# Kernel optimization log

Measured on AMD Instinct MI355X. Metric: run time of the kernel, lower is better.

Reference implementation:

```python
import jax, jax.numpy as jnp
import numpy as np

LN_EPS = 1e-5

def layer_norm(x, gamma, beta):
    mu = jnp.mean(x, axis=-1, keepdims=True)
    var = jnp.mean(jnp.square(x - mu), axis=-1, keepdims=True)
    return (x - mu) * jax.lax.rsqrt(var + LN_EPS) * gamma + beta

def setup_inputs() -> dict:
    key = jax.random.key(0)
    ks = jax.random.split(key, 10)
    B, C, N = 8, 256, 4096
    s = 1.0 / np.sqrt(C)
    inp = {
        "x": jax.random.normal(ks[0], (B, C, N), dtype=jnp.float32),
        "W_qkv": jax.random.uniform(ks[1], (C, C), jnp.float32, -s, s),            # Linear(dim, dim, bias=False)
        "W_mlp": jax.random.uniform(ks[2], (2 * C, 2 * C), jnp.float32, -0.5 * s, 0.5 * s),
        "b_mlp": jax.random.uniform(ks[3], (2 * C,), jnp.float32, -0.5 * s, 0.5 * s),
        "g1": jnp.ones((4 * C,), jnp.float32),
        "beta1": jnp.zeros((4 * C,), jnp.float32),
        "W_res": jax.random.uniform(ks[4], (C, 4 * C), jnp.float32, -0.25 * s, 0.25 * s),  # Linear(4*dim, dim, bias=False)
        "g2": jnp.ones((C,), jnp.float32),
        "beta2": jnp.zeros((C,), jnp.float32),
    }
    return inp

def reference(x, W_qkv, W_mlp, b_mlp, g1, beta1, W_res, g2, beta2):
    # x: (B, C, N) channels-first -> (B, N, C)
    NITER = 2  # niter_heads
    x = jnp.swapaxes(x, 1, 2)
    x = x @ W_qkv.T                                   # shared_qkv, (B, N, C)
    v = jax.lax.stop_gradient(x)                      # x.clone().detach()
    for _ in range(NITER):
        # first_context = x^T @ v : (B, C, C)
        ctx = jnp.einsum('bnc,bnd->bcd', x, v)
        out = jax.nn.softmax(x, axis=-1) @ ctx        # (B, N, C)
        cat1 = jnp.concatenate([out, v], axis=-1)     # (B, N, 2C)
        mlp = jax.nn.relu(cat1 @ W_mlp.T + b_mlp)     # (B, N, 2C)
        cat2 = jnp.concatenate([cat1, mlp], axis=-1)  # (B, N, 4C)
        # dropout layers are identity in eval mode
        v = layer_norm(cat2, g1, beta1) @ W_res.T + x # residual_mlp + skip
        v = layer_norm(x + v, g2, beta2)
    return jnp.swapaxes(v, 1, 2)                      # back to (B, C, N)
```

## Files before the change

kernel.cpp:

```cpp
#include <hip/hip_runtime.h>
#include <cstdint>
#include <cstddef>


using u16 = unsigned short;
using short8 = __attribute__((ext_vector_type(8))) short;
using bf16x8 = __attribute__((ext_vector_type(8))) __bf16;
using f32x4  = __attribute__((ext_vector_type(4))) float;
using i32x4  = __attribute__((ext_vector_type(4))) int;
using u16x4  = __attribute__((ext_vector_type(4))) u16;
using u16x8  = __attribute__((ext_vector_type(8))) u16;

__device__ __forceinline__ float b2f(u16 u) {
    union { unsigned u32; float f; } c; c.u32 = ((unsigned)u) << 16; return c.f;
}
__device__ __forceinline__ u16 f2b(float f) {
    union { float f; unsigned u; } c; c.f = f;
    unsigned r = c.u + 0x7FFFu + ((c.u >> 16) & 1u);
    return (u16)(r >> 16);
}
__device__ __forceinline__ void cvt(u16 a,  u16& o)   { o = a; }
__device__ __forceinline__ void cvt(float a, u16& o)  { o = f2b(a); }
__device__ __forceinline__ void cvt(float a, float& o){ o = a; }
__device__ __forceinline__ void cvt(u16 a,  float& o) { o = b2f(a); }

template<int MODE, int TRF>
__global__ __launch_bounds__(512)
void gemm_bt(const u16* __restrict__ A, const u16* __restrict__ A2,
             const u16* __restrict__ A3,
             int lda, int lda2, int lda3, int kSplit,
             const u16* __restrict__ B, int ldb, long strA, long strB,
             int statStride, int kChunk, int nKsplit,
             float* __restrict__ outF, u16* __restrict__ outB,
             long sOF, long sOB, int ldo,
             const u16* __restrict__ Xres,
             const float* __restrict__ bias,
             const float2* __restrict__ stats,
             const float* __restrict__ g, const float* __restrict__ be)
{
    __shared__ short lsA[128 * 72];
    __shared__ short lsB[128 * 72];

    const int bz    = blockIdx.z;
    const int batch = bz / nKsplit;
    const int ks    = bz - batch * nKsplit;
    const u16* Ab = A + (size_t)batch * strA;
    const u16* Bb = B + (size_t)batch * strB;
    const int colBase = blockIdx.x * 128;
    const int rowBase = blockIdx.y * 128;
    const int k0 = ks * kChunk;
    const int k1 = k0 + kChunk;

    const int t    = threadIdx.x;
    const int sRow = t >> 3;
    const int sKq  = (t & 7) << 3;

    const int lane = t & 63;
    const int w    = t >> 6;
    const int wr   = (w >> 1) * 32;
    const int wc   = (w & 1) * 64;
    const int mrow = lane & 15;
    const int q    = lane >> 4;

    float2 st0 = {0.f, 0.f}, st1 = {0.f, 0.f};
    if (TRF == 1 || TRF == 2) {
        const int sb = batch * statStride + rowBase;
        st0 = stats[sb + sRow];
        st1 = stats[sb + sRow + 64];
    }

    auto loadRaw = [&](int rloc, int kn) -> i32x4 {
        const int arow = rowBase + rloc + sRow;
        if (TRF == 2) {
            const u16* s; int ld; int kl;
            const int kc = kn + sKq;
            const int reg = kc >> 8;
            if (reg == 0)      { s = A;  ld = lda;  kl = kc; }
            else if (reg == 1) { s = A2; ld = lda2; kl = kc - 256; }
            else               { s = A3; ld = lda3; kl = kc - 512; }
            return *(const i32x4*)(s + (size_t)arow * ld + kl);
        } else if (TRF == 3) {
            const int kc = kn + sKq;
            if (kc < kSplit)
                return *(const i32x4*)(Ab + (size_t)arow * lda + kc);
            return *(const i32x4*)(A2 + (size_t)arow * lda2 + (kc - kSplit));
        }
        return *(const i32x4*)(Ab + (size_t)arow * lda + kn + sKq);
    };
    auto xform = [&](i32x4 raw, float2 st, int kn) -> i32x4 {
        if (TRF == 0 || TRF == 3) return raw;
        short8 h = __builtin_bit_cast(short8, raw);
        short8 o;
#pragma unroll
        for (int i = 0; i < 8; i++) {
            float v = b2f((u16)h[i]);
            if (TRF == 1) v = __expf(v - st.x) * st.y;
            else          v = (v - st.x) * st.y * g[kn + sKq + i] + be[kn + sKq + i];
            o[i] = (short)f2b(v);
        }
        return __builtin_bit_cast(i32x4, o);
    };

    const f32x4 fzero = {0.f, 0.f, 0.f, 0.f};
    f32x4 acc[2][4];
#pragma unroll
    for (int i = 0; i < 2; i++)
#pragma unroll
        for (int j = 0; j < 4; j++) acc[i][j] = fzero;

    const u16* pB0 = Bb + (size_t)(colBase + sRow) * ldb + sKq;
    const u16* pB1 = pB0 + (size_t)64 * ldb;

    i32x4 a0 = xform(loadRaw(0,  k0), st0, k0);
    i32x4 a1 = xform(loadRaw(64, k0), st1, k0);
    i32x4 b0 = *(const i32x4*)(pB0 + k0);
    i32x4 b1 = *(const i32x4*)(pB1 + k0);

    for (int kk = k0; kk < k1; kk += 64) {
        __syncthreads();
        *(i32x4*)&lsA[sRow * 72 + sKq]        = a0;
        *(i32x4*)&lsA[(sRow + 64) * 72 + sKq] = a1;
        *(i32x4*)&lsB[sRow * 72 + sKq]        = b0;
        *(i32x4*)&lsB[(sRow + 64) * 72 + sKq] = b1;
        __syncthreads();
        const int kn = kk + 64;
        if (kn < k1) {
            a0 = xform(loadRaw(0,  kn), st0, kn);
            a1 = xform(loadRaw(64, kn), st1, kn);
            b0 = *(const i32x4*)(pB0 + kn);
            b1 = *(const i32x4*)(pB1 + kn);
        }
#pragma unroll
        for (int h = 0; h < 2; h++) {
            bf16x8 af[2], bfr[4];
#pragma unroll
            for (int mi = 0; mi < 2; mi++)
                af[mi] = __builtin_bit_cast(bf16x8,
                    *(const short8*)&lsA[(wr + mi * 16 + mrow) * 72 + h * 32 + q * 8]);
#pragma unroll
            for (int ni = 0; ni < 4; ni++)
                bfr[ni] = __builtin_bit_cast(bf16x8,
                    *(const short8*)&lsB[(wc + ni * 16 + mrow) * 72 + h * 32 + q * 8]);
#pragma unroll
            for (int mi = 0; mi < 2; mi++)
#pragma unroll
                for (int ni = 0; ni < 4; ni++)
                    acc[mi][ni] = __builtin_amdgcn_mfma_f32_16x16x32_bf16(
                        af[mi], bfr[ni], acc[mi][ni], 0, 0, 0);
        }
    }

#pragma unroll
    for (int mi = 0; mi < 2; mi++) {
#pragma unroll
        for (int ni = 0; ni < 4; ni++) {
            const int col = colBase + wc + ni * 16 + mrow;
#pragma unroll
            for (int r = 0; r < 4; r++) {
                const int row = rowBase + wr + mi * 16 + q * 4 + r;
                float v = acc[mi][ni][r];
                if (MODE == 0) {
                    outB[(size_t)batch * sOB + (size_t)row * ldo + col] = f2b(v);
                } else if (MODE == 1) {
                    outF[((size_t)batch * nKsplit + ks) * sOF
                         + (size_t)row * ldo + col] = v;
                } else if (MODE == 3) {
                    v += bias[col];
                    v = v > 0.f ? v : 0.f;
                    outB[(size_t)row * ldo + col] = f2b(v);
                } else if (MODE == 4) {
                    v += 2.f * b2f(Xres[(size_t)row * 256 + col]);
                    outB[(size_t)row * ldo + col] = f2b(v);
                }
            }
        }
    }
}

template<typename TIN, typename TOUT>
__global__ __launch_bounds__(256)
void transpose_k(const TIN* __restrict__ in, TOUT* __restrict__ out,
                 int R, int Cc, long sIn, long sOut)
{
    __shared__ TOUT tile[32][33];
    const int b = blockIdx.z;
    const TIN* ib = in + (size_t)b * sIn;
    TOUT* ob = out + (size_t)b * sOut;
    const int c0 = blockIdx.x * 32, r0 = blockIdx.y * 32;
    const int tx = threadIdx.x & 31, ty = threadIdx.x >> 5;
#pragma unroll
    for (int i = 0; i < 32; i += 8)
        cvt(ib[(size_t)(r0 + ty + i) * Cc + c0 + tx], tile[ty + i][tx]);
    __syncthreads();
#pragma unroll
    for (int i = 0; i < 32; i += 8)
        ob[(size_t)(c0 + ty + i) * R + r0 + tx] = tile[tx][ty + i];
}

__global__ __launch_bounds__(256)
void smstats_k(const u16* __restrict__ Xb, float2* __restrict__ st)
{
    const int wave = threadIdx.x >> 6, lane = threadIdx.x & 63;
    const size_t row = (size_t)blockIdx.x * 4 + wave;
    const u16x4 xb = *(const u16x4*)(Xb + row * 256 + lane * 4);
    const float x0 = b2f(xb.x), x1 = b2f(xb.y), x2 = b2f(xb.z), x3 = b2f(xb.w);
    float m = fmaxf(fmaxf(x0, x1), fmaxf(x2, x3));
    for (int o = 32; o > 0; o >>= 1) m = fmaxf(m, __shfl_xor(m, o));
    float s = __expf(x0 - m) + __expf(x1 - m) + __expf(x2 - m) + __expf(x3 - m);
    for (int o = 32; o > 0; o >>= 1) s += __shfl_xor(s, o);
    if (lane == 0) st[row] = make_float2(m, 1.f / s);
}

__global__ __launch_bounds__(256)
void stats1024_k(const u16* __restrict__ OUT, const u16* __restrict__ V,
                 const u16* __restrict__ MLPo, float2* __restrict__ st)
{
    const int wave = threadIdx.x >> 6, lane = threadIdx.x & 63;
    const size_t row = (size_t)blockIdx.x * 4 + wave;
    const int c = lane * 16;
    const u16* src;
    if (c < 256)       src = OUT  + row * 256 + c;
    else if (c < 512)  src = V    + row * 256 + (c - 256);
    else               src = MLPo + row * 512 + (c - 512);
    short8 r0 = *(const short8*)(src);
    short8 r1 = *(const short8*)(src + 8);
    float s = 0.f, s2 = 0.f;
#pragma unroll
    for (int i = 0; i < 8; i++) {
        const float a = b2f((u16)r0[i]), b = b2f((u16)r1[i]);
        s += a + b; s2 += a * a + b * b;
    }
    for (int o = 32; o > 0; o >>= 1) { s += __shfl_xor(s, o); s2 += __shfl_xor(s2, o); }
    const float mean = s * (1.f / 1024.f);
    const float var  = s2 * (1.f / 1024.f) - mean * mean;
    if (lane == 0) st[row] = make_float2(mean, rsqrtf(var + 1e-5f));
}

template<typename OUTT, bool WRITE_VB>
__global__ __launch_bounds__(256)
void ln256t_k(const u16* __restrict__ Tb, const float* __restrict__ g,
              const float* __restrict__ be, u16* __restrict__ Vb,
              OUTT* __restrict__ outT)
{
    constexpr int STRIDE = (sizeof(OUTT) == 2) ? 266 : 261;
    __shared__ OUTT tile[32 * STRIDE];
    const int wid = threadIdx.x >> 6, lane = threadIdx.x & 63;
    const int bx = blockIdx.x;
    const size_t r0 = (size_t)bx * 32;
    const int b  = bx >> 7;
    const int n0 = (bx & 127) * 32;

#pragma unroll
    for (int j = 0; j < 8; j++) {
        const int lr = wid * 8 + j;
        const size_t row = r0 + lr;
        const u16x4 tb = *(const u16x4*)(Tb + row * 256 + lane * 4);
        const float x0 = b2f(tb.x), x1 = b2f(tb.y), x2 = b2f(tb.z), x3 = b2f(tb.w);
        float s  = x0 + x1 + x2 + x3;
        float s2 = x0 * x0 + x1 * x1 + x2 * x2 + x3 * x3;
        for (int o = 32; o > 0; o >>= 1) { s += __shfl_xor(s, o); s2 += __shfl_xor(s2, o); }
        const float mean = s * (1.f / 256.f);
        const float var  = s2 * (1.f / 256.f) - mean * mean;
        const float rstd = rsqrtf(var + 1e-5f);
        const int c = lane * 4;
        float4 ov = { (x0 - mean) * rstd * g[c + 0] + be[c + 0],
                      (x1 - mean) * rstd * g[c + 1] + be[c + 1],
                      (x2 - mean) * rstd * g[c + 2] + be[c + 2],
                      (x3 - mean) * rstd * g[c + 3] + be[c + 3] };
        if (WRITE_VB) {
            u16x4 vb = { f2b(ov.x), f2b(ov.y), f2b(ov.z), f2b(ov.w) };
            *(u16x4*)(Vb + row * 256 + c) = vb;
        }
        OUTT* tl = &tile[lr * STRIDE + c];
        cvt(ov.x, tl[0]); cvt(ov.y, tl[1]); cvt(ov.z, tl[2]); cvt(ov.w, tl[3]);
    }
    __syncthreads();

    const int c = threadIdx.x;
    OUTT* dst = outT + ((size_t)b * 256 + c) * 4096 + n0;
    if (sizeof(OUTT) == 2) {
#pragma unroll
        for (int k = 0; k < 4; k++) {
            u16x8 v;
#pragma unroll
            for (int i = 0; i < 8; i++) v[i] = *(const u16*)&tile[(k * 8 + i) * STRIDE + c];
            *(u16x8*)((u16*)dst + k * 8) = v;
        }
    } else {
#pragma unroll
        for (int k = 0; k < 8; k++) {
            float4 v;
            v.x = *(const float*)&tile[(k * 4 + 0) * STRIDE + c];
            v.y = *(const float*)&tile[(k * 4 + 1) * STRIDE + c];
            v.z = *(const float*)&tile[(k * 4 + 2) * STRIDE + c];
            v.w = *(const float*)&tile[(k * 4 + 3) * STRIDE + c];
            *(float4*)((float*)dst + k * 4) = v;
        }
    }
}

__global__ __launch_bounds__(256)
void ctxreduce_k(const float* __restrict__ ctxp, u16* __restrict__ ctxb)
{
    const int i = blockIdx.x * 256 + threadIdx.x;
    const int batch  = i >> 14;
    const int within = i & 16383;
    const float4* src = (const float4*)ctxp + (size_t)batch * 16 * 16384 + within;
    float4 s = {0.f, 0.f, 0.f, 0.f};
#pragma unroll
    for (int ks = 0; ks < 16; ks++) {
        const float4 v = src[(size_t)ks * 16384];
        s.x += v.x; s.y += v.y; s.z += v.z; s.w += v.w;
    }
    u16x4 o = { f2b(s.x), f2b(s.y), f2b(s.z), f2b(s.w) };
    ((u16x4*)ctxb)[i] = o;
}

__global__ __launch_bounds__(256)
void wconv_k(const float* __restrict__ Wq, const float* __restrict__ Wm,
             const float* __restrict__ Wr, u16* __restrict__ oq,
             u16* __restrict__ om, u16* __restrict__ orr)
{
    const int i = blockIdx.x * 256 + threadIdx.x;
    const float* src; u16* dst; int j;
    if (i < 16384)      { src = Wq; dst = oq;  j = i; }
    else if (i < 81920) { src = Wm; dst = om;  j = i - 16384; }
    else                { src = Wr; dst = orr; j = i - 81920; }
    const float4 v = ((const float4*)src)[j];
    u16x4 o = { f2b(v.x), f2b(v.y), f2b(v.z), f2b(v.w) };
    ((u16x4*)dst)[j] = o;
}

extern "C" void kernel_launch(void* const* d_in, const int* in_sizes, int n_in,
                              void* d_out, int out_size, void* d_ws, size_t ws_size,
                              hipStream_t stream)
{
    (void)in_sizes; (void)n_in; (void)out_size; (void)ws_size;
    const float* x    = (const float*)d_in[0];
    const float* Wqkv = (const float*)d_in[1];
    const float* Wmlp = (const float*)d_in[2];
    const float* bmlp = (const float*)d_in[3];
    const float* g1   = (const float*)d_in[4];
    const float* be1  = (const float*)d_in[5];
    const float* Wres = (const float*)d_in[6];
    const float* g2   = (const float*)d_in[7];
    const float* be2  = (const float*)d_in[8];

    char* ws = (char*)d_ws;
    u16*    Xb   = (u16*)ws;    ws += (size_t)16777216;
    u16*    XT   = (u16*)ws;    ws += (size_t)16777216;
    u16*    Vb   = (u16*)ws;    ws += (size_t)16777216;
    u16*    VT2  = (u16*)ws;    ws += (size_t)16777216;
    u16*    OUT  = (u16*)ws;    ws += (size_t)16777216;
    u16*    MLPo = (u16*)ws;    ws += (size_t)33554432;
    u16*    Tb   = (u16*)ws;    ws += (size_t)16777216;
    float*  ctxp = (float*)ws;  ws += (size_t)33554432;
    u16*    ctxb = (u16*)ws;    ws += (size_t)1048576;
    float2* smst = (float2*)ws; ws += (size_t)262144;
    float2* lnst = (float2*)ws; ws += (size_t)262144;
    u16*    Wq_b = (u16*)ws;    ws += (size_t)131072;
    u16*    Wm_b = (u16*)ws;    ws += (size_t)524288;
    u16*    Wr_b = (u16*)ws;    ws += (size_t)524288;
    u16*    xt   = MLPo;

    wconv_k<<<dim3(576), 256, 0, stream>>>(Wqkv, Wmlp, Wres, Wq_b, Wm_b, Wr_b);

    transpose_k<float, u16><<<dim3(128, 8, 8), 256, 0, stream>>>(
        x, xt, 256, 4096, 256L * 4096, 4096L * 256);

    gemm_bt<0, 0><<<dim3(2, 256, 1), 512, 0, stream>>>(
        xt, nullptr, nullptr, 256, 0, 0, 0, Wq_b, 256, 0, 0, 0, 256, 1,
        nullptr, Xb, 0, 0, 256, nullptr, nullptr, nullptr, nullptr, nullptr);

    transpose_k<u16, u16><<<dim3(8, 128, 8), 256, 0, stream>>>(
        Xb, XT, 4096, 256, 4096L * 256, 256L * 4096);

    const u16* VTcur = XT;
    const u16* Vcur  = Xb;

    for (int it = 0; it < 2; ++it) {
        smstats_k<<<dim3(8192), 256, 0, stream>>>(Xb, smst);

        gemm_bt<1, 0><<<dim3(2, 2, 128), 512, 0, stream>>>(
            VTcur, nullptr, nullptr, 4096, 0, 0, 0, XT, 4096,
            1048576, 1048576, 0, 256, 16,
            ctxp, nullptr, 65536, 0, 256, nullptr, nullptr, nullptr, nullptr, nullptr);
        ctxreduce_k<<<dim3(512), 256, 0, stream>>>(ctxp, ctxb);

        gemm_bt<0, 1><<<dim3(2, 32, 8), 512, 0, stream>>>(
            Xb, nullptr, nullptr, 256, 0, 0, 0, ctxb, 256,
            1048576, 65536, 4096, 256, 1,
            nullptr, OUT, 0, 1048576, 256, nullptr, nullptr, smst, nullptr, nullptr);

        gemm_bt<3, 3><<<dim3(4, 256, 1), 512, 0, stream>>>(
            OUT, Vcur, nullptr, 256, 256, 0, 256, Wm_b, 512, 0, 0, 0, 512, 1,
            nullptr, MLPo, 0, 0, 512, nullptr, bmlp, nullptr, nullptr, nullptr);

        stats1024_k<<<dim3(8192), 256, 0, stream>>>(OUT, Vcur, MLPo, lnst);

        gemm_bt<4, 2><<<dim3(2, 256, 1), 512, 0, stream>>>(
            OUT, Vcur, MLPo, 256, 256, 512, 0, Wr_b, 1024, 0, 0, 0, 1024, 1,
            nullptr, Tb, 0, 0, 256, Xb, nullptr, lnst, g1, be1);

        if (it == 0) {
            ln256t_k<u16, true><<<dim3(1024), 256, 0, stream>>>(
                Tb, g2, be2, Vb, VT2);
            VTcur = VT2;
            Vcur  = Vb;
        } else {
            ln256t_k<float, false><<<dim3(1024), 256, 0, stream>>>(
                Tb, g2, be2, nullptr, (float*)d_out);
        }
    }
}
```

Measured before the change: 385.3 us.

## Fold LayerNorm gamma/beta into W_res and apply normalization in GEMM epilogue

The first LayerNorm is moved out of the A-operand load path of the residual GEMM. Gamma is folded into W_res, and the row sums of W_res*gamma and W_res*beta are precomputed in a new prep kernel. The epilogue then applies rstd*(acc - mean*sum_g) + bias_b, so the GEMM reads raw bf16 activations with no per-element normalization or per-element gamma/beta loads in the inner loop. The catch is that mean subtraction now happens after accumulation, which can cost precision when the mean is large relative to the variance. The kernel still reads g and be in the epilogue, but they now hold the precomputed row sums.

```diff
diff --git a/kernel.cpp b/kernel.cpp
--- a/kernel.cpp
+++ b/kernel.cpp
@@ -63,7 +63,7 @@
     const int q    = lane >> 4;
 
     float2 st0 = {0.f, 0.f}, st1 = {0.f, 0.f};
-    if (TRF == 1 || TRF == 2) {
+    if (TRF == 1) {
         const int sb = batch * statStride + rowBase;
         st0 = stats[sb + sRow];
         st1 = stats[sb + sRow + 64];
@@ -87,15 +87,14 @@
         }
         return *(const i32x4*)(Ab + (size_t)arow * lda + kn + sKq);
     };
-    auto xform = [&](i32x4 raw, float2 st, int kn) -> i32x4 {
-        if (TRF == 0 || TRF == 3) return raw;
+    auto xform = [&](i32x4 raw, float2 st) -> i32x4 {
+        if (TRF != 1) return raw;
         short8 h = __builtin_bit_cast(short8, raw);
         short8 o;
 #pragma unroll
         for (int i = 0; i < 8; i++) {
             float v = b2f((u16)h[i]);
-            if (TRF == 1) v = __expf(v - st.x) * st.y;
-            else          v = (v - st.x) * st.y * g[kn + sKq + i] + be[kn + sKq + i];
+            v = __expf(v - st.x) * st.y;
             o[i] = (short)f2b(v);
         }
         return __builtin_bit_cast(i32x4, o);
@@ -111,8 +110,8 @@
     const u16* pB0 = Bb + (size_t)(colBase + sRow) * ldb + sKq;
     const u16* pB1 = pB0 + (size_t)64 * ldb;
 
-    i32x4 a0 = xform(loadRaw(0,  k0), st0, k0);
-    i32x4 a1 = xform(loadRaw(64, k0), st1, k0);
+    i32x4 a0 = xform(loadRaw(0,  k0), st0);
+    i32x4 a1 = xform(loadRaw(64, k0), st1);
     i32x4 b0 = *(const i32x4*)(pB0 + k0);
     i32x4 b1 = *(const i32x4*)(pB1 + k0);
 
@@ -125,8 +124,8 @@
         __syncthreads();
         const int kn = kk + 64;
         if (kn < k1) {
-            a0 = xform(loadRaw(0,  kn), st0, kn);
-            a1 = xform(loadRaw(64, kn), st1, kn);
+            a0 = xform(loadRaw(0,  kn), st0);
+            a1 = xform(loadRaw(64, kn), st1);
             b0 = *(const i32x4*)(pB0 + kn);
             b1 = *(const i32x4*)(pB1 + kn);
         }
@@ -169,7 +168,9 @@
                     v = v > 0.f ? v : 0.f;
                     outB[(size_t)row * ldo + col] = f2b(v);
                 } else if (MODE == 4) {
-                    v += 2.f * b2f(Xres[(size_t)row * 256 + col]);
+                    const float2 ln = stats[row];
+                    v = ln.y * (v - ln.x * g[col]) + be[col]
+                        + 2.f * b2f(Xres[(size_t)row * 256 + col]);
                     outB[(size_t)row * ldo + col] = f2b(v);
                 }
             }
@@ -318,17 +319,40 @@
 
 __global__ __launch_bounds__(256)
 void wconv_k(const float* __restrict__ Wq, const float* __restrict__ Wm,
-             const float* __restrict__ Wr, u16* __restrict__ oq,
-             u16* __restrict__ om, u16* __restrict__ orr)
+             u16* __restrict__ oq, u16* __restrict__ om)
 {
     const int i = blockIdx.x * 256 + threadIdx.x;
     const float* src; u16* dst; int j;
-    if (i < 16384)      { src = Wq; dst = oq;  j = i; }
-    else if (i < 81920) { src = Wm; dst = om;  j = i - 16384; }
-    else                { src = Wr; dst = orr; j = i - 81920; }
+    if (i < 16384) { src = Wq; dst = oq; j = i; }
+    else           { src = Wm; dst = om; j = i - 16384; }
     const float4 v = ((const float4*)src)[j];
     u16x4 o = { f2b(v.x), f2b(v.y), f2b(v.z), f2b(v.w) };
     ((u16x4*)dst)[j] = o;
+}
+
+__global__ __launch_bounds__(256)
+void wresprep_k(const float* __restrict__ Wres, const float* __restrict__ g1,
+                const float* __restrict__ be1, u16* __restrict__ Wr_b,
+                float* __restrict__ sg, float* __restrict__ br)
+{
+    const int wv = threadIdx.x >> 6, lane = threadIdx.x & 63;
+    const int row = blockIdx.x * 4 + wv;
+    const float* src = Wres + (size_t)row * 1024;
+    float s = 0.f, b = 0.f;
+#pragma unroll
+    for (int j = 0; j < 4; j++) {
+        const int c = j * 256 + lane * 4;
+        const float4 w  = *(const float4*)(src + c);
+        const float4 gg = *(const float4*)(g1 + c);
+        const float4 bb = *(const float4*)(be1 + c);
+        const float4 wg = { w.x * gg.x, w.y * gg.y, w.z * gg.z, w.w * gg.w };
+        u16x4 o = { f2b(wg.x), f2b(wg.y), f2b(wg.z), f2b(wg.w) };
+        *(u16x4*)(Wr_b + (size_t)row * 1024 + c) = o;
+        s += wg.x + wg.y + wg.z + wg.w;
+        b += w.x * bb.x + w.y * bb.y + w.z * bb.z + w.w * bb.w;
+    }
+    for (int o = 32; o > 0; o >>= 1) { s += __shfl_xor(s, o); b += __shfl_xor(b, o); }
+    if (lane == 0) { sg[row] = s; br[row] = b; }
 }
 
 extern "C" void kernel_launch(void* const* d_in, const int* in_sizes, int n_in,
@@ -361,9 +385,12 @@
     u16*    Wq_b = (u16*)ws;    ws += (size_t)131072;
     u16*    Wm_b = (u16*)ws;    ws += (size_t)524288;
     u16*    Wr_b = (u16*)ws;    ws += (size_t)524288;
+    float*  sg   = (float*)ws;  ws += (size_t)1024;
+    float*  br   = (float*)ws;  ws += (size_t)1024;
     u16*    xt   = MLPo;
 
-    wconv_k<<<dim3(576), 256, 0, stream>>>(Wqkv, Wmlp, Wres, Wq_b, Wm_b, Wr_b);
+    wconv_k<<<dim3(320), 256, 0, stream>>>(Wqkv, Wmlp, Wq_b, Wm_b);
+    wresprep_k<<<dim3(64), 256, 0, stream>>>(Wres, g1, be1, Wr_b, sg, br);
 
     transpose_k<float, u16><<<dim3(128, 8, 8), 256, 0, stream>>>(
         x, xt, 256, 4096, 256L * 4096, 4096L * 256);
@@ -400,7 +427,7 @@
 
         gemm_bt<4, 2><<<dim3(2, 256, 1), 512, 0, stream>>>(
             OUT, Vcur, MLPo, 256, 256, 512, 0, Wr_b, 1024, 0, 0, 0, 1024, 1,
-            nullptr, Tb, 0, 0, 256, Xb, nullptr, lnst, g1, be1);
+            nullptr, Tb, 0, 0, 256, Xb, nullptr, lnst, sg, br);
 
         if (it == 0) {
             ln256t_k<u16, true><<<dim3(1024), 256, 0, stream>>>(
```

After: 374.8 us. -2.7%, faster.
